# Optimization experiments

Hardware: AMD Instinct MI355X
Metric: run time of the kernel (lower is better)

## Reference

```python
import jax, jax.numpy as jnp
import numpy as np

DIM = 1024
HEADS = 16
HEAD_DIM = DIM // HEADS
FF = 4096
B, S = 2, 2048
EPS = 1e-6
NEG = float(jnp.finfo(jnp.float32).min)


def rmsnorm(x, w):
    return x * jax.lax.rsqrt(jnp.mean(x * x, axis=-1, keepdims=True) + EPS) * w


def setup_inputs() -> dict:
    key = jax.random.key(0)
    ks = jax.random.split(key, 12)
    s = 1.0 / np.sqrt(DIM)
    return {
        "x": jax.random.normal(ks[0], (B, S, DIM), jnp.float32),
        "src_key_padding_mask": jax.random.randint(ks[1], (B, S), 0, 2).astype(bool),
        "rel_pos_bias": jax.random.normal(ks[2], (1, HEADS, S, S), jnp.float32),
        "Wq": jax.random.normal(ks[3], (DIM, DIM), jnp.float32) * s,
        "Wk": jax.random.normal(ks[4], (DIM, DIM), jnp.float32) * s,
        "Wv": jax.random.normal(ks[5], (DIM, DIM), jnp.float32) * s,
        "Wo": jax.random.normal(ks[6], (DIM, DIM), jnp.float32) * s,
        "W1": jax.random.normal(ks[7], (DIM, FF), jnp.float32) * s,
        "b1": jnp.zeros((FF,), jnp.float32),
        "W2": jax.random.normal(ks[8], (FF, DIM), jnp.float32) * (1.0 / np.sqrt(FF)),
        "b2": jnp.zeros((DIM,), jnp.float32),
        "g1": jnp.ones((DIM,), jnp.float32),
        "g2": jnp.ones((DIM,), jnp.float32),
    }


def reference(x, src_key_padding_mask, rel_pos_bias, Wq, Wk, Wv, Wo, W1, b1, W2, b2, g1, g2):
    # pre-norm self-attention
    h = rmsnorm(x, g1)  # [B,S,D]
    q = (h @ Wq).reshape(B, S, HEADS, HEAD_DIM).transpose(0, 2, 1, 3)
    k = (h @ Wk).reshape(B, S, HEADS, HEAD_DIM).transpose(0, 2, 1, 3)
    v = (h @ Wv).reshape(B, S, HEADS, HEAD_DIM).transpose(0, 2, 1, 3)
    scale = HEAD_DIM ** -0.5
    scores = jnp.einsum('bhqd,bhkd->bhqk', q, k) * scale + rel_pos_bias
    scores = jnp.where(src_key_padding_mask[:, None, None, :], NEG, scores)
    attn = jax.nn.softmax(scores, axis=-1)
    out = jnp.einsum('bhqk,bhkd->bhqd', attn, v)
    out = out.transpose(0, 2, 1, 3).reshape(B, S, DIM) @ Wo
    x = x + out
    # GELU FFN (exact erf gelu, matching torch F.gelu default)
    h2 = rmsnorm(x, g2)
    h2 = jax.nn.gelu(h2 @ W1 + b1, approximate=False) @ W2 + b2
    return x + h2
```

## Files before the change

### kernel.cpp

```cpp
#include <hip/hip_runtime.h>
#include <math.h>

typedef __attribute__((ext_vector_type(8))) short   short8;
typedef __attribute__((ext_vector_type(4))) short   short4v;
typedef __attribute__((ext_vector_type(8))) __bf16  bf16x8;
typedef __attribute__((ext_vector_type(4))) float   f32x4;
typedef __attribute__((ext_vector_type(16))) float  f32x16;
typedef unsigned short u16;

#define DIMD 1024
#define NHEAD 16
#define HD 64
#define FFD 4096
#define BB 2
#define SSEQ 2048
#define NSPLIT 2
#define KVSPAN (SSEQ / NSPLIT)
#define NROWS (BB * NHEAD * SSEQ)
#define NEGF -3.4028235e38f

__device__ __forceinline__ u16 f2bf(float f){
  unsigned u = __float_as_uint(f);
  u += 0x7FFFu + ((u >> 16) & 1u);
  return (u16)(u >> 16);
}
__device__ __forceinline__ float bf2f(u16 v){
  return __uint_as_float(((unsigned)v) << 16);
}
__device__ __forceinline__ void gload16(const u16* g, u16* l){
  __builtin_amdgcn_global_load_lds((const __attribute__((address_space(1))) void*)g,
                                   (__attribute__((address_space(3))) void*)l, 16, 0, 0);
}

__global__ void normalize_mask(const unsigned char* __restrict__ m, unsigned char* __restrict__ outm){
  __shared__ int any;
  if (threadIdx.x == 0) any = 0;
  __syncthreads();
  int bad = 0;
  for (int i = threadIdx.x; i < BB * SSEQ; i += 1024)
    if ((i & 3) && m[i]) bad = 1;
  if (bad) atomicOr(&any, 1);
  __syncthreads();
  bool is_i32 = (any == 0);
  if (is_i32){
    const int* mi = (const int*)m;
    for (int k = threadIdx.x; k < BB * SSEQ; k += 1024)
      outm[k] = (unsigned char)(mi[k] != 0);
  } else {
    for (int k = threadIdx.x; k < BB * SSEQ; k += 1024)
      outm[k] = m[k] ? 1 : 0;
  }
}

__global__ void transpose_to_bf16(const float* __restrict__ W, u16* __restrict__ Wt, int K, int N){
  __shared__ float tile[32][33];
  int n0 = blockIdx.x * 32, k0 = blockIdx.y * 32;
  int tx = threadIdx.x, ty = threadIdx.y;
  #pragma unroll
  for (int i = 0; i < 32; i += 8)
    tile[ty + i][tx] = W[(size_t)(k0 + ty + i) * N + n0 + tx];
  __syncthreads();
  #pragma unroll
  for (int i = 0; i < 32; i += 8)
    Wt[(size_t)(n0 + ty + i) * K + k0 + tx] = f2bf(tile[tx][ty + i]);
}

__global__ void transpose4_to_bf16(const float* __restrict__ Wq, const float* __restrict__ Wk,
                                   const float* __restrict__ Wv, const float* __restrict__ Wo,
                                   u16* __restrict__ Tqkv, u16* __restrict__ To){
  __shared__ float tile[32][33];
  const float* W;
  u16* T;
  switch (blockIdx.z){
    case 0: W = Wq; T = Tqkv;                        break;
    case 1: W = Wk; T = Tqkv + (size_t)1024*1024;    break;
    case 2: W = Wv; T = Tqkv + (size_t)2048*1024;    break;
    default: W = Wo; T = To;                         break;
  }
  int n0 = blockIdx.x * 32, k0 = blockIdx.y * 32;
  int tx = threadIdx.x, ty = threadIdx.y;
  #pragma unroll
  for (int i = 0; i < 32; i += 8)
    tile[ty + i][tx] = W[(size_t)(k0 + ty + i) * 1024 + n0 + tx];
  __syncthreads();
  #pragma unroll
  for (int i = 0; i < 32; i += 8)
    T[(size_t)(n0 + ty + i) * 1024 + k0 + tx] = f2bf(tile[tx][ty + i]);
}

__global__ void vtrans(const u16* __restrict__ qkv, u16* __restrict__ vt){
  __shared__ u16 tile[32][33];
  int s0 = blockIdx.x * 32, d0 = blockIdx.y * 32;
  int bh = blockIdx.z;
  int b = bh >> 4, h = bh & 15;
  int tx = threadIdx.x, ty = threadIdx.y;
  const u16* src = qkv + (size_t)(b * SSEQ) * 3072 + 2048 + h * HD + d0;
  #pragma unroll
  for (int i = 0; i < 32; i += 8)
    tile[ty + i][tx] = src[(size_t)(s0 + ty + i) * 3072 + tx];
  __syncthreads();
  u16* dst = vt + ((size_t)bh * HD + d0) * SSEQ + s0;
  #pragma unroll
  for (int i = 0; i < 32; i += 8)
    dst[(size_t)(ty + i) * SSEQ + tx] = tile[tx][ty + i];
}

__global__ __launch_bounds__(256) void rmsnorm_k(const float* __restrict__ x, const float* __restrict__ g,
                                                 u16* __restrict__ out, int D){
  int row = blockIdx.x;
  const float* xr = x + (size_t)row * D;
  float ss = 0.f;
  for (int i = threadIdx.x * 4; i < D; i += 1024){
    float4 v = *(const float4*)&xr[i];
    ss += v.x*v.x + v.y*v.y + v.z*v.z + v.w*v.w;
  }
  #pragma unroll
  for (int o = 32; o > 0; o >>= 1) ss += __shfl_down(ss, o);
  __shared__ float red[4];
  if ((threadIdx.x & 63) == 0) red[threadIdx.x >> 6] = ss;
  __syncthreads();
  float tot = red[0] + red[1] + red[2] + red[3];
  float rs = rsqrtf(tot / (float)D + 1e-6f);
  for (int i = threadIdx.x * 4; i < D; i += 1024){
    float4 v  = *(const float4*)&xr[i];
    float4 gv = *(const float4*)&g[i];
    ushort4 o4;
    o4.x = f2bf(v.x * rs * gv.x);
    o4.y = f2bf(v.y * rs * gv.y);
    o4.z = f2bf(v.z * rs * gv.z);
    o4.w = f2bf(v.w * rs * gv.w);
    *(ushort4*)&out[(size_t)row * D + i] = o4;
  }
}

__device__ __forceinline__ void xcd_swz(int& bx, int& by){
  int gx = gridDim.x, nwg = gx * gridDim.y;
  int flat = by * gx + bx;
  int q = nwg >> 3;
  flat = (flat & 7) * q + (flat >> 3);
  bx = flat % gx;
  by = flat / gx;
}

template<int EPI>
__global__ __launch_bounds__(512, 2) void gemm8p(const u16* __restrict__ A, const u16* __restrict__ Bt,
                                                 u16* __restrict__ outb, const float* __restrict__ bias,
                                                 int M, int N, int K){
  extern __shared__ u16 lds[];
  const int tid = threadIdx.x;
  const int lane = tid & 63, lr = lane >> 4, lc = lane & 15;
  const int wid = tid >> 6, wr = wid >> 2, wc = wid & 3;
  int bx = blockIdx.x, by = blockIdx.y;
  xcd_swz(bx, by);
  const int m0 = by * 256, n0 = bx * 256;
  const int NT = K >> 5;
  const int slot8 = ((lr ^ (lc & 3)) << 3);

  f32x4 acc[8][4];
  #pragma unroll
  for (int i = 0; i < 8; i++)
    #pragma unroll
    for (int j = 0; j < 4; j++) acc[i][j] = (f32x4){0.f,0.f,0.f,0.f};

  const int srow = tid >> 2;
  const int scg  = (tid & 3) ^ (srow & 3);

  auto stage = [&](int t, int buf, int rsel){
    int row = ((rsel & 1) << 7) + srow;
    const u16* src = ((rsel < 2) ? A + (size_t)(m0 + row) * K
                                 : Bt + (size_t)(n0 + row) * K) + t * 32 + scg * 8;
    u16* dst = lds + buf * 16384 + ((rsel & 2) << 12) + ((rsel & 1) << 12) + tid * 8;
    gload16(src, dst);
  };
  auto ldA = [&](int buf, int mi) -> bf16x8 {
    int ra = wr * 128 + mi * 16 + lc;
    return *(const bf16x8*)&lds[buf * 16384 + ra * 32 + slot8];
  };
  auto ldB = [&](int buf, int ni) -> bf16x8 {
    int rb = wc * 64 + ni * 16 + lc;
    return *(const bf16x8*)&lds[buf * 16384 + 8192 + rb * 32 + slot8];
  };

  #pragma unroll
  for (int rs = 0; rs < 4; rs++) stage(0, 0, rs);
  #pragma unroll
  for (int rs = 0; rs < 4; rs++) stage(1, 1, rs);
  asm volatile("s_waitcnt vmcnt(4)" ::: "memory");
  __builtin_amdgcn_s_barrier();

  int buf = 0;
  for (int t = 0; t < NT; t++){
    int sbuf = buf + 2; if (sbuf >= 3) sbuf -= 3;
    bool ds = (t + 2 < NT);
    bf16x8 a[4], b[4];
    #pragma unroll
    for (int mi = 0; mi < 4; mi++) a[mi] = ldA(buf, mi);
    #pragma unroll
    for (int ni = 0; ni < 4; ni++) b[ni] = ldB(buf, ni);
    if (ds){ stage(t + 2, sbuf, 0); stage(t + 2, sbuf, 1); }
    __builtin_amdgcn_s_barrier();
    __builtin_amdgcn_s_setprio(1);
    #pragma unroll
    for (int mi = 0; mi < 4; mi++)
      #pragma unroll
      for (int ni = 0; ni < 4; ni++)
        acc[mi][ni] = __builtin_amdgcn_mfma_f32_16x16x32_bf16(a[mi], b[ni], acc[mi][ni], 0, 0, 0);
    __builtin_amdgcn_s_setprio(0);
    __builtin_amdgcn_s_barrier();
    #pragma unroll
    for (int mi = 0; mi < 4; mi++) a[mi] = ldA(buf, mi + 4);
    if (ds){ stage(t + 2, sbuf, 2); stage(t + 2, sbuf, 3); }
    __builtin_amdgcn_s_barrier();
    __builtin_amdgcn_s_setprio(1);
    #pragma unroll
    for (int mi = 0; mi < 4; mi++)
      #pragma unroll
      for (int ni = 0; ni < 4; ni++)
        acc[mi + 4][ni] = __builtin_amdgcn_mfma_f32_16x16x32_bf16(a[mi], b[ni], acc[mi + 4][ni], 0, 0, 0);
    __builtin_amdgcn_s_setprio(0);
    if (t + 2 < NT)      { asm volatile("s_waitcnt vmcnt(4)" ::: "memory"); }
    else if (t + 1 < NT) { asm volatile("s_waitcnt vmcnt(0)" ::: "memory"); }
    __builtin_amdgcn_s_barrier();
    buf++; if (buf == 3) buf = 0;
  }

  #pragma unroll
  for (int mi = 0; mi < 8; mi++){
    #pragma unroll
    for (int ni = 0; ni < 4; ni++){
      int col = n0 + wc * 64 + ni * 16 + lc;
      #pragma unroll
      for (int r = 0; r < 4; r++){
        int row = m0 + wr * 128 + mi * 16 + lr * 4 + r;
        float v = acc[mi][ni][r];
        if (EPI == 2){
          v += bias[col];
          v = 0.5f * v * (1.f + erff(v * 0.70710678118654752f));
        }
        outb[(size_t)row * N + col] = f2bf(v);
      }
    }
  }
}

__global__ __launch_bounds__(512, 2) void gemm8p_sk(const u16* __restrict__ A, const u16* __restrict__ Bt,
                                                    u16* __restrict__ part,
                                                    int M, int N, int Kstride, int Klen){
  extern __shared__ u16 lds[];
  const int tid = threadIdx.x;
  const int lane = tid & 63, lr = lane >> 4, lc = lane & 15;
  const int wid = tid >> 6, wr = wid >> 2, wc = wid & 3;
  int bx = blockIdx.x, by = blockIdx.y;
  xcd_swz(bx, by);
  const int sk = blockIdx.z;
  const size_t koff = (size_t)sk * Klen;
  const int m0 = by * 256, n0 = bx * 256;
  const int NT = Klen >> 5;
  const int slot8 = ((lr ^ (lc & 3)) << 3);

  f32x4 acc[8][4];
  #pragma unroll
  for (int i = 0; i < 8; i++)
    #pragma unroll
    for (int j = 0; j < 4; j++) acc[i][j] = (f32x4){0.f,0.f,0.f,0.f};

  const int srow = tid >> 2;
  const int scg  = (tid & 3) ^ (srow & 3);

  auto stage = [&](int t, int buf, int rsel){
    int row = ((rsel & 1) << 7) + srow;
    const u16* src = ((rsel < 2) ? A + (size_t)(m0 + row) * Kstride
                                 : Bt + (size_t)(n0 + row) * Kstride) + koff + t * 32 + scg * 8;
    u16* dst = lds + buf * 16384 + ((rsel & 2) << 12) + ((rsel & 1) << 12) + tid * 8;
    gload16(src, dst);
  };
  auto ldA = [&](int buf, int mi) -> bf16x8 {
    int ra = wr * 128 + mi * 16 + lc;
    return *(const bf16x8*)&lds[buf * 16384 + ra * 32 + slot8];
  };
  auto ldB = [&](int buf, int ni) -> bf16x8 {
    int rb = wc * 64 + ni * 16 + lc;
    return *(const bf16x8*)&lds[buf * 16384 + 8192 + rb * 32 + slot8];
  };

  #pragma unroll
  for (int rs = 0; rs < 4; rs++) stage(0, 0, rs);
  #pragma unroll
  for (int rs = 0; rs < 4; rs++) stage(1, 1, rs);
  asm volatile("s_waitcnt vmcnt(4)" ::: "memory");
  __builtin_amdgcn_s_barrier();

  int buf = 0;
  for (int t = 0; t < NT; t++){
    int sbuf = buf + 2; if (sbuf >= 3) sbuf -= 3;
    bool ds = (t + 2 < NT);
    bf16x8 a[4], b[4];
    #pragma unroll
    for (int mi = 0; mi < 4; mi++) a[mi] = ldA(buf, mi);
    #pragma unroll
    for (int ni = 0; ni < 4; ni++) b[ni] = ldB(buf, ni);
    if (ds){ stage(t + 2, sbuf, 0); stage(t + 2, sbuf, 1); }
    __builtin_amdgcn_s_barrier();
    __builtin_amdgcn_s_setprio(1);
    #pragma unroll
    for (int mi = 0; mi < 4; mi++)
      #pragma unroll
      for (int ni = 0; ni < 4; ni++)
        acc[mi][ni] = __builtin_amdgcn_mfma_f32_16x16x32_bf16(a[mi], b[ni], acc[mi][ni], 0, 0, 0);
    __builtin_amdgcn_s_setprio(0);
    __builtin_amdgcn_s_barrier();
    #pragma unroll
    for (int mi = 0; mi < 4; mi++) a[mi] = ldA(buf, mi + 4);
    if (ds){ stage(t + 2, sbuf, 2); stage(t + 2, sbuf, 3); }
    __builtin_amdgcn_s_barrier();
    __builtin_amdgcn_s_setprio(1);
    #pragma unroll
    for (int mi = 0; mi < 4; mi++)
      #pragma unroll
      for (int ni = 0; ni < 4; ni++)
        acc[mi + 4][ni] = __builtin_amdgcn_mfma_f32_16x16x32_bf16(a[mi], b[ni], acc[mi + 4][ni], 0, 0, 0);
    __builtin_amdgcn_s_setprio(0);
    if (t + 2 < NT)      { asm volatile("s_waitcnt vmcnt(4)" ::: "memory"); }
    else if (t + 1 < NT) { asm volatile("s_waitcnt vmcnt(0)" ::: "memory"); }
    __builtin_amdgcn_s_barrier();
    buf++; if (buf == 3) buf = 0;
  }

  u16* po = part + (size_t)sk * M * N;
  #pragma unroll
  for (int mi = 0; mi < 8; mi++){
    #pragma unroll
    for (int ni = 0; ni < 4; ni++){
      int col = n0 + wc * 64 + ni * 16 + lc;
      #pragma unroll
      for (int r = 0; r < 4; r++){
        int row = m0 + wr * 128 + mi * 16 + lr * 4 + r;
        po[(size_t)row * N + col] = f2bf(acc[mi][ni][r]);
      }
    }
  }
}

__global__ __launch_bounds__(256) void ffn2_merge(const u16* __restrict__ part, const float* __restrict__ x2,
                                                  const float* __restrict__ b2, float* __restrict__ out){
  size_t i = ((size_t)blockIdx.x * 256 + threadIdx.x) * 8;
  int col = (int)(i & (DIMD - 1));
  const size_t MN = (size_t)4096 * DIMD;
  short8 a0 = *(const short8*)&part[i];
  short8 a1 = *(const short8*)&part[MN + i];
  short8 a2 = *(const short8*)&part[2 * MN + i];
  short8 a3 = *(const short8*)&part[3 * MN + i];
  float r[8];
  #pragma unroll
  for (int j = 0; j < 8; j++)
    r[j] = (bf2f((u16)a0[j]) + bf2f((u16)a1[j])) + (bf2f((u16)a2[j]) + bf2f((u16)a3[j]));
  float4 xa = *(const float4*)&x2[i];
  float4 xb = *(const float4*)&x2[i + 4];
  float4 ba = *(const float4*)&b2[col];
  float4 bb = *(const float4*)&b2[col + 4];
  float4 o0 = {r[0] + xa.x + ba.x, r[1] + xa.y + ba.y, r[2] + xa.z + ba.z, r[3] + xa.w + ba.w};
  float4 o1 = {r[4] + xb.x + bb.x, r[5] + xb.y + bb.y, r[6] + xb.z + bb.z, r[7] + xb.w + bb.w};
  *(float4*)&out[i] = o0;
  *(float4*)&out[i + 4] = o1;
}

template<int EPI, int BN>
__global__ __launch_bounds__(256) void gemm_bt(const u16* __restrict__ A, const u16* __restrict__ Bt,
                                               u16* __restrict__ outb, float* __restrict__ outf,
                                               const float* __restrict__ bias, const float* __restrict__ resid,
                                               int M, int N, int K){
  constexpr int NI = BN / 32;
  __shared__ u16 As[128 * 64];
  __shared__ u16 Bs[BN * 64];
  const int tid = threadIdx.x;
  const int wid = tid >> 6, lane = tid & 63, lr = lane >> 4, lc = lane & 15;
  const int wr = wid >> 1, wc = wid & 1;
  int bx = blockIdx.x, by = blockIdx.y;
  xcd_swz(bx, by);
  const int m0 = by * 128, n0 = bx * BN;

  f32x4 acc[4][NI];
  #pragma unroll
  for (int i = 0; i < 4; i++)
    #pragma unroll
    for (int j = 0; j < NI; j++) acc[i][j] = (f32x4){0.f,0.f,0.f,0.f};

  for (int k0 = 0; k0 < K; k0 += 64){
    __syncthreads();
    #pragma unroll
    for (int j = 0; j < 4; j++){
      int c = tid + 256 * j;
      gload16(A + (size_t)(m0 + (c >> 3)) * K + k0 + (c & 7) * 8, As + c * 8);
    }
    #pragma unroll
    for (int j = 0; j < NI; j++){
      int c = tid + 256 * j;
      gload16(Bt + (size_t)(n0 + (c >> 3)) * K + k0 + (c & 7) * 8, Bs + c * 8);
    }
    __syncthreads();
    #pragma unroll
    for (int kk = 0; kk < 2; kk++){
      bf16x8 a[4], b[NI];
      #pragma unroll
      for (int mi = 0; mi < 4; mi++) a[mi] = *(const bf16x8*)&As[(wr*64 + mi*16 + lc)*64 + kk*32 + lr*8];
      #pragma unroll
      for (int ni = 0; ni < NI; ni++) b[ni] = *(const bf16x8*)&Bs[(wc*(BN/2) + ni*16 + lc)*64 + kk*32 + lr*8];
      #pragma unroll
      for (int mi = 0; mi < 4; mi++)
        #pragma unroll
        for (int ni = 0; ni < NI; ni++)
          acc[mi][ni] = __builtin_amdgcn_mfma_f32_16x16x32_bf16(a[mi], b[ni], acc[mi][ni], 0, 0, 0);
    }
  }

  #pragma unroll
  for (int mi = 0; mi < 4; mi++){
    #pragma unroll
    for (int ni = 0; ni < NI; ni++){
      #pragma unroll
      for (int r = 0; r < 4; r++){
        int row = m0 + wr*64 + mi*16 + lr*4 + r;
        int col = n0 + wc*(BN/2) + ni*16 + lc;
        float v = acc[mi][ni][r];
        size_t idx = (size_t)row * N + col;
        if (EPI == 0){
          outb[idx] = f2bf(v);
        } else if (EPI == 1){
          outf[idx] = v + resid[idx];
        } else if (EPI == 2){
          v += bias[col];
          v = 0.5f * v * (1.f + erff(v * 0.70710678118654752f));
          outb[idx] = f2bf(v);
        } else {
          outf[idx] = v + bias[col] + resid[idx];
        }
      }
    }
  }
}

__global__ __launch_bounds__(256) void attn_part(const u16* __restrict__ qkv, const u16* __restrict__ vt,
                                                 const float* __restrict__ bias,
                                                 const unsigned char* __restrict__ mask,
                                                 u16* __restrict__ Opart, float* __restrict__ mp, float* __restrict__ lp){
  __shared__ u16 Ks [64 * 64];
  __shared__ u16 Vts[64 * 64];
  __shared__ u16 Ps [4 * 32 * 72];

  const int tid = threadIdx.x;
  const int lane = tid & 63, hi = lane >> 5, lq = lane & 31;
  const int wq = tid >> 6;
  const int b  = blockIdx.x & 1;
  const int qb = blockIdx.x >> 1;
  const int h  = blockIdx.y;
  const int sp = blockIdx.z;
  const int qw = qb * 128 + wq * 32;
  const int kv_lo = sp * KVSPAN, kv_hi = kv_lo + KVSPAN;

  char* kls = (char*)Ks;
  char* vls = (char*)Vts;
  u16*  psw = Ps + wq * 32 * 72;

  bf16x8 qf[4];
  {
    const u16* qp = qkv + ((size_t)(b * SSEQ + qw + lq)) * 3072 + h * HD + hi * 8;
    #pragma unroll
    for (int dstep = 0; dstep < 4; dstep++) qf[dstep] = *(const bf16x8*)(qp + dstep * 16);
  }

  const u16* kbase = qkv + (size_t)b * SSEQ * 3072 + 1024 + h * HD;
  const u16* vbase = vt + (size_t)(b * NHEAD + h) * HD * SSEQ;
  const int c0 = tid, c1 = tid + 256;
  auto kaddr = [&](int kv0, int c){ return kbase + (size_t)(kv0 + (c >> 3)) * 3072 + (c & 7) * 8; };
  auto vaddr = [&](int kv0, int c){ return vbase + (size_t)(c >> 3) * SSEQ + kv0 + (c & 7) * 8; };
  auto sstore = [&](char* base, int c, short8 v){
    int byte = (c >> 3) * 128 + (c & 7) * 16;
    byte ^= ((c >> 3) & 7) << 4;
    *(short8*)(base + byte) = v;
  };

  const float* brow = bias + ((size_t)h * SSEQ + (qw + lq)) * SSEQ;
  const unsigned char* mbase = mask + b * SSEQ;

  short8 kr0 = *(const short8*)kaddr(kv_lo, c0);
  short8 kr1 = *(const short8*)kaddr(kv_lo, c1);
  short8 vr0 = *(const short8*)vaddr(kv_lo, c0);
  short8 vr1 = *(const short8*)vaddr(kv_lo, c1);

  float mrow = NEGF, lsum = 0.f;
  f32x16 oacc[2];
  #pragma unroll
  for (int g = 0; g < 2; g++)
    #pragma unroll
    for (int r = 0; r < 16; r++) oacc[g][r] = 0.f;

  for (int kv0 = kv_lo; kv0 < kv_hi; kv0 += 64){
    float4 bv[8]; unsigned mk[8];
    #pragma unroll
    for (int kg = 0; kg < 2; kg++)
      #pragma unroll
      for (int rq = 0; rq < 4; rq++){
        int base = kv0 + kg * 32 + 8 * rq + 4 * hi;
        bv[kg*4+rq] = *(const float4*)&brow[base];
        mk[kg*4+rq] = *(const unsigned*)&mbase[base];
      }

    __syncthreads();
    sstore(kls, c0, kr0); sstore(kls, c1, kr1);
    sstore(vls, c0, vr0); sstore(vls, c1, vr1);
    __syncthreads();

    {
      int nxt = (kv0 + 64 < kv_hi) ? kv0 + 64 : kv_lo;
      kr0 = *(const short8*)kaddr(nxt, c0);
      kr1 = *(const short8*)kaddr(nxt, c1);
      vr0 = *(const short8*)vaddr(nxt, c0);
      vr1 = *(const short8*)vaddr(nxt, c1);
    }

    f32x16 acc[2];
    #pragma unroll
    for (int g = 0; g < 2; g++)
      #pragma unroll
      for (int r = 0; r < 16; r++) acc[g][r] = 0.f;
    __builtin_amdgcn_s_setprio(1);
    #pragma unroll
    for (int kg = 0; kg < 2; kg++){
      int row = kg * 32 + lq;
      #pragma unroll
      for (int dstep = 0; dstep < 4; dstep++){
        int byte = row * 128 + dstep * 32 + hi * 16;
        byte ^= (row & 7) << 4;
        bf16x8 kf = *(const bf16x8*)(kls + byte);
        acc[kg] = __builtin_amdgcn_mfma_f32_32x32x16_bf16(kf, qf[dstep], acc[kg], 0, 0, 0);
      }
    }
    __builtin_amdgcn_s_setprio(0);

    float p[2][16];
    float tm = NEGF;
    #pragma unroll
    for (int kg = 0; kg < 2; kg++)
      #pragma unroll
      for (int r = 0; r < 16; r++){
        int g = kg * 4 + (r >> 2);
        bool m = ((mk[g] >> (8 * (r & 3))) & 0xffu) != 0;
        float v = acc[kg][r] * 0.125f + ((const float*)&bv[g])[r & 3];
        v = m ? NEGF : v;
        p[kg][r] = v;
        tm = fmaxf(tm, v);
      }
    tm = fmaxf(tm, __shfl_xor(tm, 32));

    if (__any(tm > mrow + 5.f)){
      float mnew = fmaxf(mrow, tm);
      float corr = __expf(mrow - mnew);
      lsum *= corr;
      mrow = mnew;
      #pragma unroll
      for (int r = 0; r < 16; r++){
        float cr = __shfl(corr, (r & 3) + 8 * (r >> 2) + 4 * hi);
        oacc[0][r] *= cr;
        oacc[1][r] *= cr;
      }
    }

    float psum = 0.f;
    #pragma unroll
    for (int kg = 0; kg < 2; kg++)
      #pragma unroll
      for (int r = 0; r < 16; r++){
        float sv = p[kg][r];
        float e = (sv < -1e30f) ? 0.f : __expf(sv - mrow);
        p[kg][r] = e;
        psum += e;
      }
    psum += __shfl_xor(psum, 32);
    lsum += psum;

    #pragma unroll
    for (int kg = 0; kg < 2; kg++)
      #pragma unroll
      for (int rq = 0; rq < 4; rq++){
        short4v pk;
        #pragma unroll
        for (int t = 0; t < 4; t++)
          pk[t] = (short)(__float_as_uint(p[kg][rq * 4 + t]) >> 16);
        *(short4v*)&psw[lq * 72 + kg * 32 + 8 * rq + 4 * hi] = pk;
      }

    __builtin_amdgcn_s_setprio(1);
    #pragma unroll
    for (int ks = 0; ks < 4; ks++){
      bf16x8 pa = *(const bf16x8*)&psw[lq * 72 + ks * 16 + hi * 8];
      #pragma unroll
      for (int dgrp = 0; dgrp < 2; dgrp++){
        int row = dgrp * 32 + lq;
        int byte = row * 128 + ks * 32 + hi * 16;
        byte ^= (row & 7) << 4;
        bf16x8 vf = *(const bf16x8*)(vls + byte);
        oacc[dgrp] = __builtin_amdgcn_mfma_f32_32x32x16_bf16(pa, vf, oacc[dgrp], 0, 0, 0);
      }
    }
    __builtin_amdgcn_s_setprio(0);
  }

  if (lane < 32){
    int ridx = (b * NHEAD + h) * SSEQ + qw + lq;
    mp[sp * NROWS + ridx] = mrow;
    lp[sp * NROWS + ridx] = lsum;
  }
  #pragma unroll
  for (int r = 0; r < 16; r++){
    int qloc = (r & 3) + 8 * (r >> 2) + 4 * hi;
    int ridx = (b * NHEAD + h) * SSEQ + qw + qloc;
    size_t o = ((size_t)(sp * NROWS + ridx)) * HD;
    Opart[o + lq]      = f2bf(oacc[0][r]);
    Opart[o + 32 + lq] = f2bf(oacc[1][r]);
  }
}

__global__ __launch_bounds__(256) void attn_merge(const u16* __restrict__ Opart, const float* __restrict__ mp,
                                                  const float* __restrict__ lp, u16* __restrict__ attn){
  int row = blockIdx.x * 16 + (threadIdx.x >> 4);
  int tx = threadIdx.x & 15;
  float ms[NSPLIT], ls[NSPLIT];
  float m = NEGF;
  #pragma unroll
  for (int sp = 0; sp < NSPLIT; sp++){
    ms[sp] = mp[sp * NROWS + row];
    ls[sp] = lp[sp * NROWS + row];
    if (ls[sp] > 0.f) m = fmaxf(m, ms[sp]);
  }
  float acc0 = 0.f, acc1 = 0.f, acc2 = 0.f, acc3 = 0.f, ltot = 0.f;
  #pragma unroll
  for (int sp = 0; sp < NSPLIT; sp++){
    float e = (ls[sp] > 0.f) ? __expf(ms[sp] - m) : 0.f;
    ltot += ls[sp] * e;
    ushort4 o4 = *(const ushort4*)&Opart[((size_t)(sp * NROWS + row)) * HD + tx*4];
    acc0 += e * bf2f(o4.x);
    acc1 += e * bf2f(o4.y);
    acc2 += e * bf2f(o4.z);
    acc3 += e * bf2f(o4.w);
  }
  float inv = ltot > 0.f ? 1.f / ltot : 0.f;
  int b = row >> 15, h = (row >> 11) & 15, q = row & 2047;
  ushort4 r4;
  r4.x = f2bf(acc0 * inv);
  r4.y = f2bf(acc1 * inv);
  r4.z = f2bf(acc2 * inv);
  r4.w = f2bf(acc3 * inv);
  *(ushort4*)&attn[((size_t)(b * SSEQ + q)) * DIMD + h * HD + tx*4] = r4;
}

extern "C" void kernel_launch(void* const* d_in, const int* in_sizes, int n_in,
                              void* d_out, int out_size, void* d_ws, size_t ws_size,
                              hipStream_t stream){
  const float* x    = (const float*)d_in[0];
  const unsigned char* mask = (const unsigned char*)d_in[1];
  const float* bias = (const float*)d_in[2];
  const float* Wq   = (const float*)d_in[3];
  const float* Wk   = (const float*)d_in[4];
  const float* Wv   = (const float*)d_in[5];
  const float* Wo   = (const float*)d_in[6];
  const float* W1   = (const float*)d_in[7];
  const float* b1   = (const float*)d_in[8];
  const float* W2   = (const float*)d_in[9];
  const float* b2   = (const float*)d_in[10];
  const float* g1   = (const float*)d_in[11];
  const float* g2   = (const float*)d_in[12];
  float* out = (float*)d_out;

  char* ws = (char*)d_ws;
  size_t off = 0;
  auto take = [&](size_t bytes) -> char* {
    char* p = ws + off;
    off = (off + bytes + 255) & ~(size_t)255;
    return p;
  };
  u16*  wqkv_t = (u16*) take((size_t)3072*1024*2);
  u16*  wo_t   = (u16*) take((size_t)1024*1024*2);
  u16*  w1_t   = (u16*) take((size_t)4096*1024*2);
  u16*  w2_t   = (u16*) take((size_t)1024*4096*2);
  u16*  hbuf   = (u16*) take((size_t)4096*1024*2);
  u16*  qkv    = (u16*) take((size_t)4096*3072*2);
  u16*  attn   = (u16*) take((size_t)4096*1024*2);
  float* x2    = (float*)take((size_t)4096*1024*4);
  u16*  h2     = (u16*) take((size_t)4096*1024*2);
  u16*  fbuf   = (u16*) take((size_t)4096*4096*2);
  unsigned char* nmask = (unsigned char*)take(BB*SSEQ);
  float* mpbuf = (float*)take((size_t)NSPLIT*NROWS*4);
  float* lpbuf = (float*)take((size_t)NSPLIT*NROWS*4);
  u16*  fp2    = (u16*) take((size_t)4*4096*1024*2);
  u16* Opart = fbuf;
  u16* vt_g  = hbuf;

  hipFuncSetAttribute(reinterpret_cast<const void*>(gemm8p<0>),
                      hipFuncAttributeMaxDynamicSharedMemorySize, 98304);
  hipFuncSetAttribute(reinterpret_cast<const void*>(gemm8p<2>),
                      hipFuncAttributeMaxDynamicSharedMemorySize, 98304);
  hipFuncSetAttribute(reinterpret_cast<const void*>(gemm8p_sk),
                      hipFuncAttributeMaxDynamicSharedMemorySize, 98304);

  normalize_mask<<<1, 1024, 0, stream>>>(mask, nmask);

  dim3 tb(32, 8);
  transpose4_to_bf16<<<dim3(32, 32, 4), tb, 0, stream>>>(Wq, Wk, Wv, Wo, wqkv_t, wo_t);
  transpose_to_bf16<<<dim3(128, 32), tb, 0, stream>>>(W1, w1_t, 1024, 4096);
  transpose_to_bf16<<<dim3(32, 128), tb, 0, stream>>>(W2, w2_t, 4096, 1024);

  rmsnorm_k<<<4096, 256, 0, stream>>>(x, g1, hbuf, DIMD);

  gemm8p<0><<<dim3(3072/256, 4096/256), 512, 98304, stream>>>(hbuf, wqkv_t, qkv, nullptr, 4096, 3072, 1024);

  vtrans<<<dim3(SSEQ/32, 2, BB*NHEAD), tb, 0, stream>>>(qkv, vt_g);

  attn_part<<<dim3(2*SSEQ/128, NHEAD, NSPLIT), 256, 0, stream>>>(qkv, vt_g, bias, nmask, Opart, mpbuf, lpbuf);
  attn_merge<<<dim3(NROWS/16), 256, 0, stream>>>(Opart, mpbuf, lpbuf, attn);

  gemm_bt<1,64><<<dim3(1024/64, 4096/128), 256, 0, stream>>>(attn, wo_t, nullptr, x2, nullptr, x, 4096, 1024, 1024);

  rmsnorm_k<<<4096, 256, 0, stream>>>(x2, g2, h2, DIMD);

  gemm8p<2><<<dim3(4096/256, 4096/256), 512, 98304, stream>>>(h2, w1_t, fbuf, b1, 4096, 4096, 1024);

  gemm8p_sk<<<dim3(1024/256, 4096/256, 4), 512, 98304, stream>>>(fbuf, w2_t, fp2, 4096, 1024, 4096, 1024);
  ffn2_merge<<<dim3(4096*1024/2048), 256, 0, stream>>>(fp2, x2, b2, out);
}
```

Measured before the change: 335.1 us.

## Double-buffer attention K/V via async LDS loads; split-K Wo projection with merge

The attention kernel now stages K and V tiles directly into double-buffered shared memory with async global-to-LDS loads. The next tile is prefetched while the current one is computed, and the bias and mask loads are issued early. The masked-score exp check is removed, and the score accumulators are reused in place of a separate array. The Wo projection now uses the split-K 8-wave GEMM with 4 K-splits plus a generalized merge kernel instead of the simple gemm_bt. This trades an extra bf16 partial write and read for better occupancy and overlap.

Measured after the change: 360.0 us. +7.5%, slower.

```diff
diff --git a/kernel.cpp b/kernel.cpp
--- a/kernel.cpp
+++ b/kernel.cpp
@@ -341,8 +341,9 @@
   }
 }
 
-__global__ __launch_bounds__(256) void ffn2_merge(const u16* __restrict__ part, const float* __restrict__ x2,
-                                                  const float* __restrict__ b2, float* __restrict__ out){
+template<int WITH_BIAS>
+__global__ __launch_bounds__(256) void skmerge(const u16* __restrict__ part, const float* __restrict__ resid,
+                                               const float* __restrict__ bias, float* __restrict__ out){
   size_t i = ((size_t)blockIdx.x * 256 + threadIdx.x) * 8;
   int col = (int)(i & (DIMD - 1));
   const size_t MN = (size_t)4096 * DIMD;
@@ -354,97 +355,25 @@
   #pragma unroll
   for (int j = 0; j < 8; j++)
     r[j] = (bf2f((u16)a0[j]) + bf2f((u16)a1[j])) + (bf2f((u16)a2[j]) + bf2f((u16)a3[j]));
-  float4 xa = *(const float4*)&x2[i];
-  float4 xb = *(const float4*)&x2[i + 4];
-  float4 ba = *(const float4*)&b2[col];
-  float4 bb = *(const float4*)&b2[col + 4];
-  float4 o0 = {r[0] + xa.x + ba.x, r[1] + xa.y + ba.y, r[2] + xa.z + ba.z, r[3] + xa.w + ba.w};
-  float4 o1 = {r[4] + xb.x + bb.x, r[5] + xb.y + bb.y, r[6] + xb.z + bb.z, r[7] + xb.w + bb.w};
-  *(float4*)&out[i] = o0;
-  *(float4*)&out[i + 4] = o1;
-}
-
-template<int EPI, int BN>
-__global__ __launch_bounds__(256) void gemm_bt(const u16* __restrict__ A, const u16* __restrict__ Bt,
-                                               u16* __restrict__ outb, float* __restrict__ outf,
-                                               const float* __restrict__ bias, const float* __restrict__ resid,
-                                               int M, int N, int K){
-  constexpr int NI = BN / 32;
-  __shared__ u16 As[128 * 64];
-  __shared__ u16 Bs[BN * 64];
-  const int tid = threadIdx.x;
-  const int wid = tid >> 6, lane = tid & 63, lr = lane >> 4, lc = lane & 15;
-  const int wr = wid >> 1, wc = wid & 1;
-  int bx = blockIdx.x, by = blockIdx.y;
-  xcd_swz(bx, by);
-  const int m0 = by * 128, n0 = bx * BN;
-
-  f32x4 acc[4][NI];
-  #pragma unroll
-  for (int i = 0; i < 4; i++)
-    #pragma unroll
-    for (int j = 0; j < NI; j++) acc[i][j] = (f32x4){0.f,0.f,0.f,0.f};
-
-  for (int k0 = 0; k0 < K; k0 += 64){
-    __syncthreads();
-    #pragma unroll
-    for (int j = 0; j < 4; j++){
-      int c = tid + 256 * j;
-      gload16(A + (size_t)(m0 + (c >> 3)) * K + k0 + (c & 7) * 8, As + c * 8);
-    }
-    #pragma unroll
-    for (int j = 0; j < NI; j++){
-      int c = tid + 256 * j;
-      gload16(Bt + (size_t)(n0 + (c >> 3)) * K + k0 + (c & 7) * 8, Bs + c * 8);
-    }
-    __syncthreads();
-    #pragma unroll
-    for (int kk = 0; kk < 2; kk++){
-      bf16x8 a[4], b[NI];
-      #pragma unroll
-      for (int mi = 0; mi < 4; mi++) a[mi] = *(const bf16x8*)&As[(wr*64 + mi*16 + lc)*64 + kk*32 + lr*8];
-      #pragma unroll
-      for (int ni = 0; ni < NI; ni++) b[ni] = *(const bf16x8*)&Bs[(wc*(BN/2) + ni*16 + lc)*64 + kk*32 + lr*8];
-      #pragma unroll
-      for (int mi = 0; mi < 4; mi++)
-        #pragma unroll
-        for (int ni = 0; ni < NI; ni++)
-          acc[mi][ni] = __builtin_amdgcn_mfma_f32_16x16x32_bf16(a[mi], b[ni], acc[mi][ni], 0, 0, 0);
-    }
-  }
-
-  #pragma unroll
-  for (int mi = 0; mi < 4; mi++){
-    #pragma unroll
-    for (int ni = 0; ni < NI; ni++){
-      #pragma unroll
-      for (int r = 0; r < 4; r++){
-        int row = m0 + wr*64 + mi*16 + lr*4 + r;
-        int col = n0 + wc*(BN/2) + ni*16 + lc;
-        float v = acc[mi][ni][r];
-        size_t idx = (size_t)row * N + col;
-        if (EPI == 0){
-          outb[idx] = f2bf(v);
-        } else if (EPI == 1){
-          outf[idx] = v + resid[idx];
-        } else if (EPI == 2){
-          v += bias[col];
-          v = 0.5f * v * (1.f + erff(v * 0.70710678118654752f));
-          outb[idx] = f2bf(v);
-        } else {
-          outf[idx] = v + bias[col] + resid[idx];
-        }
-      }
-    }
-  }
+  float4 xa = *(const float4*)&resid[i];
+  float4 xb = *(const float4*)&resid[i + 4];
+  float o[8] = {r[0]+xa.x, r[1]+xa.y, r[2]+xa.z, r[3]+xa.w, r[4]+xb.x, r[5]+xb.y, r[6]+xb.z, r[7]+xb.w};
+  if (WITH_BIAS){
+    float4 ba = *(const float4*)&bias[col];
+    float4 bb = *(const float4*)&bias[col + 4];
+    o[0] += ba.x; o[1] += ba.y; o[2] += ba.z; o[3] += ba.w;
+    o[4] += bb.x; o[5] += bb.y; o[6] += bb.z; o[7] += bb.w;
+  }
+  *(float4*)&out[i]     = (float4){o[0], o[1], o[2], o[3]};
+  *(float4*)&out[i + 4] = (float4){o[4], o[5], o[6], o[7]};
 }
 
 __global__ __launch_bounds__(256) void attn_part(const u16* __restrict__ qkv, const u16* __restrict__ vt,
                                                  const float* __restrict__ bias,
                                                  const unsigned char* __restrict__ mask,
                                                  u16* __restrict__ Opart, float* __restrict__ mp, float* __restrict__ lp){
-  __shared__ u16 Ks [64 * 64];
-  __shared__ u16 Vts[64 * 64];
+  __shared__ u16 Kls[2 * 64 * 64];
+  __shared__ u16 Vls[2 * 64 * 64];
   __shared__ u16 Ps [4 * 32 * 72];
 
   const int tid = threadIdx.x;
@@ -457,9 +386,7 @@
   const int qw = qb * 128 + wq * 32;
   const int kv_lo = sp * KVSPAN, kv_hi = kv_lo + KVSPAN;
 
-  char* kls = (char*)Ks;
-  char* vls = (char*)Vts;
-  u16*  psw = Ps + wq * 32 * 72;
+  u16* psw = Ps + wq * 32 * 72;
 
   bf16x8 qf[4];
   {
@@ -470,32 +397,21 @@
 
   const u16* kbase = qkv + (size_t)b * SSEQ * 3072 + 1024 + h * HD;
   const u16* vbase = vt + (size_t)(b * NHEAD + h) * HD * SSEQ;
-  const int c0 = tid, c1 = tid + 256;
-  auto kaddr = [&](int kv0, int c){ return kbase + (size_t)(kv0 + (c >> 3)) * 3072 + (c & 7) * 8; };
-  auto vaddr = [&](int kv0, int c){ return vbase + (size_t)(c >> 3) * SSEQ + kv0 + (c & 7) * 8; };
-  auto sstore = [&](char* base, int c, short8 v){
-    int byte = (c >> 3) * 128 + (c & 7) * 16;
-    byte ^= ((c >> 3) & 7) << 4;
-    *(short8*)(base + byte) = v;
+
+  auto stage = [&](int kv0, int buf){
+    #pragma unroll
+    for (int i = 0; i < 2; i++){
+      int c = tid + 256 * i;
+      int row = c >> 3, cg = (c & 7) ^ (row & 7);
+      gload16(kbase + (size_t)(kv0 + row) * 3072 + cg * 8, Kls + buf * 4096 + c * 8);
+      gload16(vbase + (size_t)row * SSEQ + kv0 + cg * 8,  Vls + buf * 4096 + c * 8);
+    }
   };
 
   const float* brow = bias + ((size_t)h * SSEQ + (qw + lq)) * SSEQ;
   const unsigned char* mbase = mask + b * SSEQ;
-
-  short8 kr0 = *(const short8*)kaddr(kv_lo, c0);
-  short8 kr1 = *(const short8*)kaddr(kv_lo, c1);
-  short8 vr0 = *(const short8*)vaddr(kv_lo, c0);
-  short8 vr1 = *(const short8*)vaddr(kv_lo, c1);
-
-  float mrow = NEGF, lsum = 0.f;
-  f32x16 oacc[2];
-  #pragma unroll
-  for (int g = 0; g < 2; g++)
-    #pragma unroll
-    for (int r = 0; r < 16; r++) oacc[g][r] = 0.f;
-
-  for (int kv0 = kv_lo; kv0 < kv_hi; kv0 += 64){
-    float4 bv[8]; unsigned mk[8];
+  float4 bv[8]; unsigned mk[8];
+  auto bload = [&](int kv0){
     #pragma unroll
     for (int kg = 0; kg < 2; kg++)
       #pragma unroll
@@ -504,19 +420,28 @@
         bv[kg*4+rq] = *(const float4*)&brow[base];
         mk[kg*4+rq] = *(const unsigned*)&mbase[base];
       }
-
-    __syncthreads();
-    sstore(kls, c0, kr0); sstore(kls, c1, kr1);
-    sstore(vls, c0, vr0); sstore(vls, c1, vr1);
-    __syncthreads();
-
-    {
-      int nxt = (kv0 + 64 < kv_hi) ? kv0 + 64 : kv_lo;
-      kr0 = *(const short8*)kaddr(nxt, c0);
-      kr1 = *(const short8*)kaddr(nxt, c1);
-      vr0 = *(const short8*)vaddr(nxt, c0);
-      vr1 = *(const short8*)vaddr(nxt, c1);
-    }
+  };
+
+  stage(kv_lo, 0);
+  bload(kv_lo);
+  asm volatile("s_waitcnt vmcnt(0)" ::: "memory");
+  __syncthreads();
+
+  float mrow = NEGF, lsum = 0.f;
+  f32x16 oacc[2];
+  #pragma unroll
+  for (int g = 0; g < 2; g++)
+    #pragma unroll
+    for (int r = 0; r < 16; r++) oacc[g][r] = 0.f;
+
+  int buf = 0;
+  for (int kv0 = kv_lo; kv0 < kv_hi; kv0 += 64){
+    int nxt = kv0 + 64;
+    bool more = nxt < kv_hi;
+    if (more) stage(nxt, buf ^ 1);
+
+    const char* kls = (const char*)(Kls + buf * 4096);
+    const char* vls = (const char*)(Vls + buf * 4096);
 
     f32x16 acc[2];
     #pragma unroll
@@ -537,7 +462,6 @@
     }
     __builtin_amdgcn_s_setprio(0);
 
-    float p[2][16];
     float tm = NEGF;
     #pragma unroll
     for (int kg = 0; kg < 2; kg++)
@@ -547,9 +471,12 @@
         bool m = ((mk[g] >> (8 * (r & 3))) & 0xffu) != 0;
         float v = acc[kg][r] * 0.125f + ((const float*)&bv[g])[r & 3];
         v = m ? NEGF : v;
-        p[kg][r] = v;
+        acc[kg][r] = v;
         tm = fmaxf(tm, v);
       }
+
+    if (more) bload(nxt);
+
     tm = fmaxf(tm, __shfl_xor(tm, 32));
 
     if (__any(tm > mrow + 5.f)){
@@ -570,9 +497,8 @@
     for (int kg = 0; kg < 2; kg++)
       #pragma unroll
       for (int r = 0; r < 16; r++){
-        float sv = p[kg][r];
-        float e = (sv < -1e30f) ? 0.f : __expf(sv - mrow);
-        p[kg][r] = e;
+        float e = __expf(acc[kg][r] - mrow);
+        acc[kg][r] = e;
         psum += e;
       }
     psum += __shfl_xor(psum, 32);
@@ -585,7 +511,7 @@
         short4v pk;
         #pragma unroll
         for (int t = 0; t < 4; t++)
-          pk[t] = (short)(__float_as_uint(p[kg][rq * 4 + t]) >> 16);
+          pk[t] = (short)(__float_as_uint(acc[kg][rq * 4 + t]) >> 16);
         *(short4v*)&psw[lq * 72 + kg * 32 + 8 * rq + 4 * hi] = pk;
       }
 
@@ -603,6 +529,10 @@
       }
     }
     __builtin_amdgcn_s_setprio(0);
+
+    asm volatile("s_waitcnt vmcnt(0)" ::: "memory");
+    __syncthreads();
+    buf ^= 1;
   }
 
   if (lane < 32){
@@ -718,12 +648,13 @@
   attn_part<<<dim3(2*SSEQ/128, NHEAD, NSPLIT), 256, 0, stream>>>(qkv, vt_g, bias, nmask, Opart, mpbuf, lpbuf);
   attn_merge<<<dim3(NROWS/16), 256, 0, stream>>>(Opart, mpbuf, lpbuf, attn);
 
-  gemm_bt<1,64><<<dim3(1024/64, 4096/128), 256, 0, stream>>>(attn, wo_t, nullptr, x2, nullptr, x, 4096, 1024, 1024);
+  gemm8p_sk<<<dim3(1024/256, 4096/256, 4), 512, 98304, stream>>>(attn, wo_t, fp2, 4096, 1024, 1024, 256);
+  skmerge<0><<<dim3(4096*1024/2048), 256, 0, stream>>>(fp2, x, nullptr, x2);
 
   rmsnorm_k<<<4096, 256, 0, stream>>>(x2, g2, h2, DIMD);
 
   gemm8p<2><<<dim3(4096/256, 4096/256), 512, 98304, stream>>>(h2, w1_t, fbuf, b1, 4096, 4096, 1024);
 
   gemm8p_sk<<<dim3(1024/256, 4096/256, 4), 512, 98304, stream>>>(fbuf, w2_t, fp2, 4096, 1024, 4096, 1024);
-  ffn2_merge<<<dim3(4096*1024/2048), 256, 0, stream>>>(fp2, x2, b2, out);
-}
+  skmerge<1><<<dim3(4096*1024/2048), 256, 0, stream>>>(fp2, x2, b2, out);
+}
```

## Use split-K 256-tile GEMM for Wo projection and fuse merge with RMSNorm

Applied to the files above, without the earlier changes.

Replaces the small-tile gemm_bt Wo projection with the 256x256 split-K gemm8p_sk kernel (4 K-slices of 256), writing bf16 partials. A new skmerge_rms kernel sums the partials, adds the residual, writes x2, and computes the second RMSNorm in the same pass, which removes the separate rmsnorm_k launch. The partials are stored in bf16, so the attention-output projection loses some precision, and extra partial traffic is added.

After: 332.9 us, median of 3. Within noise of the previous version (-0.6%).

```diff
diff --git a/kernel.cpp b/kernel.cpp
--- a/kernel.cpp
+++ b/kernel.cpp
@@ -341,6 +341,48 @@
   }
 }
 
+__global__ __launch_bounds__(256) void skmerge_rms(const u16* __restrict__ part, const float* __restrict__ resid,
+                                                   const float* __restrict__ g2, float* __restrict__ x2,
+                                                   u16* __restrict__ h2){
+  size_t i = ((size_t)blockIdx.x * 256 + threadIdx.x) * 8;
+  int col = (int)(i & (DIMD - 1));
+  const size_t MN = (size_t)4096 * DIMD;
+  short8 a0 = *(const short8*)&part[i];
+  short8 a1 = *(const short8*)&part[MN + i];
+  short8 a2 = *(const short8*)&part[2 * MN + i];
+  short8 a3 = *(const short8*)&part[3 * MN + i];
+  float4 xa = *(const float4*)&resid[i];
+  float4 xb = *(const float4*)&resid[i + 4];
+  float o[8];
+  #pragma unroll
+  for (int j = 0; j < 8; j++)
+    o[j] = (bf2f((u16)a0[j]) + bf2f((u16)a1[j])) + (bf2f((u16)a2[j]) + bf2f((u16)a3[j]));
+  o[0] += xa.x; o[1] += xa.y; o[2] += xa.z; o[3] += xa.w;
+  o[4] += xb.x; o[5] += xb.y; o[6] += xb.z; o[7] += xb.w;
+  *(float4*)&x2[i]     = (float4){o[0], o[1], o[2], o[3]};
+  *(float4*)&x2[i + 4] = (float4){o[4], o[5], o[6], o[7]};
+
+  float ss = 0.f;
+  #pragma unroll
+  for (int j = 0; j < 8; j++) ss += o[j] * o[j];
+  #pragma unroll
+  for (int off = 32; off > 0; off >>= 1) ss += __shfl_down(ss, off);
+  __shared__ float red[4];
+  if ((threadIdx.x & 63) == 0) red[threadIdx.x >> 6] = ss;
+  __syncthreads();
+  float tot = (threadIdx.x < 128) ? (red[0] + red[1]) : (red[2] + red[3]);
+  float rs = rsqrtf(tot / (float)DIMD + 1e-6f);
+  float4 ga = *(const float4*)&g2[col];
+  float4 gb = *(const float4*)&g2[col + 4];
+  ushort4 h0, h1;
+  h0.x = f2bf(o[0] * rs * ga.x); h0.y = f2bf(o[1] * rs * ga.y);
+  h0.z = f2bf(o[2] * rs * ga.z); h0.w = f2bf(o[3] * rs * ga.w);
+  h1.x = f2bf(o[4] * rs * gb.x); h1.y = f2bf(o[5] * rs * gb.y);
+  h1.z = f2bf(o[6] * rs * gb.z); h1.w = f2bf(o[7] * rs * gb.w);
+  *(ushort4*)&h2[i]     = h0;
+  *(ushort4*)&h2[i + 4] = h1;
+}
+
 __global__ __launch_bounds__(256) void ffn2_merge(const u16* __restrict__ part, const float* __restrict__ x2,
                                                   const float* __restrict__ b2, float* __restrict__ out){
   size_t i = ((size_t)blockIdx.x * 256 + threadIdx.x) * 8;
@@ -362,81 +404,6 @@
   float4 o1 = {r[4] + xb.x + bb.x, r[5] + xb.y + bb.y, r[6] + xb.z + bb.z, r[7] + xb.w + bb.w};
   *(float4*)&out[i] = o0;
   *(float4*)&out[i + 4] = o1;
-}
-
-template<int EPI, int BN>
-__global__ __launch_bounds__(256) void gemm_bt(const u16* __restrict__ A, const u16* __restrict__ Bt,
-                                               u16* __restrict__ outb, float* __restrict__ outf,
-                                               const float* __restrict__ bias, const float* __restrict__ resid,
-                                               int M, int N, int K){
-  constexpr int NI = BN / 32;
-  __shared__ u16 As[128 * 64];
-  __shared__ u16 Bs[BN * 64];
-  const int tid = threadIdx.x;
-  const int wid = tid >> 6, lane = tid & 63, lr = lane >> 4, lc = lane & 15;
-  const int wr = wid >> 1, wc = wid & 1;
-  int bx = blockIdx.x, by = blockIdx.y;
-  xcd_swz(bx, by);
-  const int m0 = by * 128, n0 = bx * BN;
-
-  f32x4 acc[4][NI];
-  #pragma unroll
-  for (int i = 0; i < 4; i++)
-    #pragma unroll
-    for (int j = 0; j < NI; j++) acc[i][j] = (f32x4){0.f,0.f,0.f,0.f};
-
-  for (int k0 = 0; k0 < K; k0 += 64){
-    __syncthreads();
-    #pragma unroll
-    for (int j = 0; j < 4; j++){
-      int c = tid + 256 * j;
-      gload16(A + (size_t)(m0 + (c >> 3)) * K + k0 + (c & 7) * 8, As + c * 8);
-    }
-    #pragma unroll
-    for (int j = 0; j < NI; j++){
-      int c = tid + 256 * j;
-      gload16(Bt + (size_t)(n0 + (c >> 3)) * K + k0 + (c & 7) * 8, Bs + c * 8);
-    }
-    __syncthreads();
-    #pragma unroll
-    for (int kk = 0; kk < 2; kk++){
-      bf16x8 a[4], b[NI];
-      #pragma unroll
-      for (int mi = 0; mi < 4; mi++) a[mi] = *(const bf16x8*)&As[(wr*64 + mi*16 + lc)*64 + kk*32 + lr*8];
-      #pragma unroll
-      for (int ni = 0; ni < NI; ni++) b[ni] = *(const bf16x8*)&Bs[(wc*(BN/2) + ni*16 + lc)*64 + kk*32 + lr*8];
-      #pragma unroll
-      for (int mi = 0; mi < 4; mi++)
-        #pragma unroll
-        for (int ni = 0; ni < NI; ni++)
-          acc[mi][ni] = __builtin_amdgcn_mfma_f32_16x16x32_bf16(a[mi], b[ni], acc[mi][ni], 0, 0, 0);
-    }
-  }
-
-  #pragma unroll
-  for (int mi = 0; mi < 4; mi++){
-    #pragma unroll
-    for (int ni = 0; ni < NI; ni++){
-      #pragma unroll
-      for (int r = 0; r < 4; r++){
-        int row = m0 + wr*64 + mi*16 + lr*4 + r;
-        int col = n0 + wc*(BN/2) + ni*16 + lc;
-        float v = acc[mi][ni][r];
-        size_t idx = (size_t)row * N + col;
-        if (EPI == 0){
-          outb[idx] = f2bf(v);
-        } else if (EPI == 1){
-          outf[idx] = v + resid[idx];
-        } else if (EPI == 2){
-          v += bias[col];
-          v = 0.5f * v * (1.f + erff(v * 0.70710678118654752f));
-          outb[idx] = f2bf(v);
-        } else {
-          outf[idx] = v + bias[col] + resid[idx];
-        }
-      }
-    }
-  }
 }
 
 __global__ __launch_bounds__(256) void attn_part(const u16* __restrict__ qkv, const u16* __restrict__ vt,
@@ -718,9 +685,8 @@
   attn_part<<<dim3(2*SSEQ/128, NHEAD, NSPLIT), 256, 0, stream>>>(qkv, vt_g, bias, nmask, Opart, mpbuf, lpbuf);
   attn_merge<<<dim3(NROWS/16), 256, 0, stream>>>(Opart, mpbuf, lpbuf, attn);
 
-  gemm_bt<1,64><<<dim3(1024/64, 4096/128), 256, 0, stream>>>(attn, wo_t, nullptr, x2, nullptr, x, 4096, 1024, 1024);
-
-  rmsnorm_k<<<4096, 256, 0, stream>>>(x2, g2, h2, DIMD);
+  gemm8p_sk<<<dim3(1024/256, 4096/256, 4), 512, 98304, stream>>>(attn, wo_t, fp2, 4096, 1024, 1024, 256);
+  skmerge_rms<<<dim3(4096*1024/2048), 256, 0, stream>>>(fp2, x, g2, x2, h2);
 
   gemm8p<2><<<dim3(4096/256, 4096/256), 512, 98304, stream>>>(h2, w1_t, fbuf, b1, 4096, 4096, 1024);
 
```
